# Kernel tuning notes

Measured on AMD Instinct MI355X. Metric: run time of the kernel, lower is better.

Reference implementation:

```python
import jax, jax.numpy as jnp
import numpy as np

D_MODEL = 2048
D_FFN = 8192
TOP_K = 256


def setup_inputs() -> dict:
    key = jax.random.key(0)
    kx, kg, ku, kd = jax.random.split(key, 4)
    B, S = 4, 2048
    x = jax.random.normal(kx, (B, S, D_MODEL), dtype=jnp.float32)
    # kaiming_uniform_(a=sqrt(5)) on a 2D tensor -> U(-1/sqrt(fan_in), 1/sqrt(fan_in)),
    # where PyTorch's fan_in is size(1) of the parameter.
    bg = 1.0 / np.sqrt(D_FFN)
    w_gate = jax.random.uniform(kg, (D_MODEL, D_FFN), jnp.float32, -bg, bg)
    w_up = jax.random.uniform(ku, (D_MODEL, D_FFN), jnp.float32, -bg, bg)
    bd = 1.0 / np.sqrt(D_MODEL)
    w_down = jax.random.uniform(kd, (D_FFN, D_MODEL), jnp.float32, -bd, bd)
    return {"x": x, "w_gate": w_gate, "w_up": w_up, "w_down": w_down}


def reference(x, w_gate, w_up, w_down):
    orig_shape = x.shape
    xf = x.reshape(-1, x.shape[-1])          # [N, d_model]
    G = xf @ w_gate                           # [N, d_ffn]
    U = xf @ w_up                             # [N, d_ffn]
    _, idx = jax.lax.top_k(G, TOP_K)          # [N, k] int32 indices into d_ffn
    Gk = jnp.take_along_axis(G, idx, axis=-1)  # [N, k]
    Uk = jnp.take_along_axis(U, idx, axis=-1)  # [N, k]
    Z = jax.nn.silu(Gk) * Uk                   # fused sparse SiLU activation, [N, k]
    # Sparse-to-dense down projection: scatter the k active channels per token
    # back into d_ffn (top-k indices are unique per row, so .set is exact),
    # then a single dense matmul with w_down.
    N = G.shape[0]
    Zd = jnp.zeros((N, D_FFN), dtype=Z.dtype).at[jnp.arange(N)[:, None], idx].set(Z)
    out = Zd @ w_down                          # [N, d_model]
    return out.reshape(*orig_shape[:-1], w_down.shape[-1])
```

## Files before the change

kernel.cpp:

```cpp
#include <hip/hip_runtime.h>
#include <hip/hip_bf16.h>
#include <stdint.h>

#define D_MODEL 2048
#define D_FFN   8192
#define NTOK    8192
#define TOPK    256

typedef __bf16 bf16x8 __attribute__((ext_vector_type(8)));
typedef __bf16 bf16x4 __attribute__((ext_vector_type(4)));
typedef float  f32x4  __attribute__((ext_vector_type(4)));

__device__ inline void load_lds16(const void* g, void* l) {
    __builtin_amdgcn_global_load_lds((__attribute__((address_space(1))) void*)g,
                                     (__attribute__((address_space(3))) void*)l,
                                     16, 0, 0);
}

template<int NSEG, int SEGK, int LDA, int LDB, int LDC, bool ATOMIC>
__global__ __attribute__((amdgpu_flat_work_group_size(512, 512),
                          amdgpu_waves_per_eu(2)))
void g256p(const __bf16* __restrict__ A0, const __bf16* __restrict__ A1,
           const __bf16* __restrict__ A2,
           const __bf16* __restrict__ B0, const __bf16* __restrict__ B1,
           const __bf16* __restrict__ B2,
           float* __restrict__ C)
{
    constexpr int KEXT = NSEG * SEGK;
    constexpr int NH   = KEXT / 32;
    constexpr int NIT  = NH / 4;

    __shared__ __align__(16) __bf16 sA[4][256][32];
    __shared__ __align__(16) __bf16 sB[4][256][32];

    const int tid  = threadIdx.x;
    const int lane = tid & 63;
    const int wid  = tid >> 6;
    const int mb   = blockIdx.y;
    const int nb   = blockIdx.x;

    const size_t zoff = (size_t)blockIdx.z * KEXT;
    A0 += zoff; B0 += zoff;

    const int wm = (wid >> 2) * 128;
    const int wn = (wid & 3) * 64;
    const int fr = lane & 15;
    const int q  = lane >> 4;

    const int swz8 = ((q ^ ((fr >> 1) & 3)) * 8);
    const int cl   = lane & 3;
    const int sr0  = wid * 32 + (lane >> 2);
    const int cg8a = (cl ^ ((sr0 >> 1) & 3)) * 8;

    f32x4 acc[8][4] = {};

    auto STAGE = [&](int op, int J) {
        const int s = J & 3;
        int seg = 0, kin = J * 32;
        if (NSEG > 1) { seg = (J * 32) / SEGK; kin = J * 32 - seg * SEGK; }
        const __bf16* base = op
            ? ((NSEG == 1 || seg == 0) ? B0 : (seg == 1 ? B1 : B2))
            : ((NSEG == 1 || seg == 0) ? A0 : (seg == 1 ? A1 : A2));
        const int rowbase = (op ? nb : mb) * 256;
        const int ld = op ? LDB : LDA;
        char* ldsb = (char*)(op ? &sB[s][0][0] : &sA[s][0][0]) + wid * 2048;
        #pragma unroll
        for (int p = 0; p < 2; ++p) {
            const int r = sr0 + p * 16;
            load_lds16(base + (size_t)(rowbase + r) * ld + kin + cg8a,
                       ldsb + p * 1024);
        }
    };

#define P_READ_B(s) { _Pragma("unroll") for (int ni = 0; ni < 4; ++ni) {       \
        const int r = wn + fr + ni * 16;                                       \
        bfr[ni] = *(const bf16x8*)&sB[s][r][swz8]; } }
#define P_READ_A(s, h) { _Pragma("unroll") for (int mi = 0; mi < 4; ++mi) {    \
        const int r = wm + (h) * 64 + fr + mi * 16;                            \
        af[mi] = *(const bf16x8*)&sA[s][r][swz8]; } }
#define P_MFMA(h) { __builtin_amdgcn_s_setprio(1);                             \
    _Pragma("unroll") for (int mi = 0; mi < 4; ++mi)                           \
    _Pragma("unroll") for (int ni = 0; ni < 4; ++ni)                           \
        acc[(h) * 4 + mi][ni] = __builtin_amdgcn_mfma_f32_16x16x32_bf16(       \
            af[mi], bfr[ni], acc[(h) * 4 + mi][ni], 0, 0, 0);                  \
    __builtin_amdgcn_s_setprio(0); }
#define P_STAGE2(Joff) { const int J = J0 + (Joff);                            \
        if (J >= 4 && J < NH) { STAGE(0, J); STAGE(1, J); } }
#define P_BAR  __builtin_amdgcn_s_barrier()
#define P_LGKM { asm volatile("s_waitcnt lgkmcnt(0)" ::: "memory");            \
                 __builtin_amdgcn_sched_barrier(0); }
#define SLOT_PHASE(sp, VM) {                                                   \
        P_READ_B(sp); P_READ_A(sp, 0);                                         \
        P_STAGE2(3 + (sp));                                                    \
        P_BAR; P_LGKM;                                                         \
        P_MFMA(0);                                                             \
        __builtin_amdgcn_sched_barrier(0);                                     \
        P_READ_A(sp, 1);                                                       \
        P_LGKM;                                                                \
        P_MFMA(1);                                                             \
        VM;                                                                    \
        P_BAR; }

    #pragma unroll
    for (int J = 0; J < 4; ++J) { STAGE(0, J); STAGE(1, J); }
    asm volatile("s_waitcnt vmcnt(0)" ::: "memory");
    P_BAR;

    for (int i = 0; i < NIT; ++i) {
        const int J0 = 4 * i;
        const bool last = (i == NIT - 1);
        bf16x8 af[4], bfr[4];

        SLOT_PHASE(0, );
        SLOT_PHASE(1,
            if (last) { asm volatile("s_waitcnt vmcnt(0)" ::: "memory"); }
            else      { asm volatile("s_waitcnt vmcnt(4)" ::: "memory"); });
        SLOT_PHASE(2, );
        SLOT_PHASE(3,
            if (last) { asm volatile("s_waitcnt vmcnt(0)" ::: "memory"); }
            else      { asm volatile("s_waitcnt vmcnt(4)" ::: "memory"); });
    }

#undef P_READ_B
#undef P_READ_A
#undef P_MFMA
#undef P_STAGE2
#undef P_BAR
#undef P_LGKM
#undef SLOT_PHASE

    const int orow = q * 4;
    #pragma unroll
    for (int ai = 0; ai < 8; ++ai) {
        const int rl = wm + (ai >> 2) * 64 + (ai & 3) * 16 + orow;
        #pragma unroll
        for (int ni = 0; ni < 4; ++ni)
            #pragma unroll
            for (int j = 0; j < 4; ++j) {
                const int r = mb * 256 + rl + j;
                const int c = nb * 256 + wn + ni * 16 + fr;
                if (ATOMIC)
                    unsafeAtomicAdd(&C[(size_t)r * LDC + c], acc[ai][ni][j]);
                else
                    C[(size_t)r * LDC + c] = acc[ai][ni][j];
            }
    }
}

__global__ __launch_bounds__(256)
void split_convert(const float* __restrict__ in, __bf16* __restrict__ hi,
                   __bf16* __restrict__ lo, int n4)
{
    const int i = blockIdx.x * 256 + threadIdx.x;
    if (i >= n4) return;
    const float4 v = ((const float4*)in)[i];
    float f[4] = {v.x, v.y, v.z, v.w};
    bf16x4 h, l;
    #pragma unroll
    for (int j = 0; j < 4; ++j) {
        __bf16 hb = (__bf16)f[j];
        h[j] = hb;
        l[j] = (__bf16)(f[j] - (float)hb);
    }
    ((bf16x4*)hi)[i] = h;
    ((bf16x4*)lo)[i] = l;
}

template<bool SPLIT>
__global__ __launch_bounds__(256)
void transpose_bf16(const float* __restrict__ in, __bf16* __restrict__ outHi,
                    __bf16* __restrict__ outLo, int R, int C)
{
    __shared__ float tile[32][33];
    const int bx = blockIdx.x * 32;
    const int by = blockIdx.y * 32;
    const int tx = threadIdx.x & 31;
    const int ty = threadIdx.x >> 5;
    #pragma unroll
    for (int i = 0; i < 4; ++i)
        tile[ty + 8 * i][tx] = in[(size_t)(by + ty + 8 * i) * C + (bx + tx)];
    __syncthreads();
    #pragma unroll
    for (int i = 0; i < 4; ++i) {
        const float v = tile[tx][ty + 8 * i];
        const size_t o = (size_t)(bx + ty + 8 * i) * R + (by + tx);
        const __bf16 h = (__bf16)v;
        outHi[o] = h;
        if (SPLIT) outLo[o] = (__bf16)(v - (float)h);
    }
}

#define TK_EPS 3e-5f
#define TK_MAXA 64

__global__ __launch_bounds__(256)
void topk256(const float* __restrict__ G, const float* __restrict__ xblk,
             const float* __restrict__ wgate,
             int* __restrict__ idxOut, float* __restrict__ gkOut)
{
    const int row = blockIdx.x;
    const int t = threadIdx.x;
    const int lane = t & 63;
    const int wid  = t >> 6;

    __shared__ unsigned keys[D_FFN];
    __shared__ float    xr[D_MODEL];
    __shared__ unsigned hist[256];
    __shared__ unsigned scanb[256];
    __shared__ int      sIdx[TOPK];
    __shared__ float    sVal[TOPK];
    __shared__ int      ambIdx[TK_MAXA];
    __shared__ double   ambVal[TK_MAXA];
    __shared__ double   redW[4];
    __shared__ unsigned sh_bin, sh_above, sh_nc, sh_na, sh_fill;

    const float* g = G + (size_t)row * D_FFN;
    const float* xrow = xblk + (size_t)row * D_MODEL;
    for (int i = t; i < D_FFN; i += 256) {
        const unsigned u = __float_as_uint(g[i]);
        keys[i] = (u & 0x80000000u) ? ~u : (u | 0x80000000u);
    }
    for (int i = t; i < D_MODEL; i += 256) xr[i] = xrow[i];
    if (t == 0) { sh_nc = 0; sh_na = 0; sh_fill = 0; }
    __syncthreads();

    unsigned prefix = 0, pmask = 0;
    int remaining = TOPK;
    for (int shift = 24; shift >= 0; shift -= 8) {
        hist[t] = 0;
        __syncthreads();
        for (int i = t; i < D_FFN; i += 256) {
            const unsigned k = keys[i];
            if ((k & pmask) == prefix) atomicAdd(&hist[(k >> shift) & 255u], 1u);
        }
        __syncthreads();
        scanb[t] = hist[t];
        __syncthreads();
        for (int off = 1; off < 256; off <<= 1) {
            const unsigned add = (t + off < 256) ? scanb[t + off] : 0u;
            __syncthreads();
            scanb[t] += add;
            __syncthreads();
        }
        const unsigned above = (t == 255) ? 0u : scanb[t + 1];
        if (scanb[t] >= (unsigned)remaining && above < (unsigned)remaining) {
            sh_bin = (unsigned)t;
            sh_above = above;
        }
        __syncthreads();
        prefix |= sh_bin << shift;
        pmask  |= 0xFFu << shift;
        remaining -= (int)sh_above;
        __syncthreads();
    }
    const unsigned Tkey = prefix;
    const float vT = __uint_as_float((Tkey & 0x80000000u) ? (Tkey & 0x7FFFFFFFu) : ~Tkey);

    for (int i = t; i < D_FFN; i += 256) {
        const unsigned k = keys[i];
        const float f = __uint_as_float((k & 0x80000000u) ? (k & 0x7FFFFFFFu) : ~k);
        if (f > vT + TK_EPS) {
            const unsigned p = atomicAdd(&sh_nc, 1u);
            sIdx[p] = i;
            sVal[p] = f;
        } else if (f >= vT - TK_EPS) {
            const unsigned p = atomicAdd(&sh_na, 1u);
            if (p < TK_MAXA) ambIdx[p] = i;
        }
    }
    __syncthreads();
    const int nc = (int)sh_nc;
    const int na = min((int)sh_na, TK_MAXA);
    const int need = TOPK - nc;

    if (need >= na) {
        if (t < na) {
            const unsigned k = keys[ambIdx[t]];
            sIdx[nc + t] = ambIdx[t];
            sVal[nc + t] = __uint_as_float((k & 0x80000000u) ? (k & 0x7FFFFFFFu) : ~k);
        }
        __syncthreads();
    } else {
        for (int j = 0; j < na; ++j) {
            const int col = ambIdx[j];
            double p = 0.0;
            for (int k = t; k < D_MODEL; k += 256)
                p += (double)xr[k] * (double)wgate[(size_t)k * D_FFN + col];
            #pragma unroll
            for (int o = 32; o > 0; o >>= 1) p += __shfl_xor(p, o, 64);
            if (lane == 0) redW[wid] = p;
            __syncthreads();
            if (t == 0) ambVal[j] = (redW[0] + redW[1]) + (redW[2] + redW[3]);
            __syncthreads();
        }
        if (t < na) {
            const double v = ambVal[t];
            const int    c = ambIdx[t];
            int r = 0;
            for (int j = 0; j < na; ++j) {
                const double vj = ambVal[j];
                if (vj > v || (vj == v && ambIdx[j] < c)) r++;
            }
            if (r < need) {
                const unsigned p = atomicAdd(&sh_fill, 1u);
                sIdx[nc + p] = c;
                sVal[nc + p] = (float)v;
            }
        }
        __syncthreads();
    }

    idxOut[(size_t)row * TOPK + t] = sIdx[t];
    gkOut[(size_t)row * TOPK + t] = sVal[t];
}

__global__ __launch_bounds__(256)
void z_fused(const int* __restrict__ idx, const float* __restrict__ gk,
             const float* __restrict__ U, __bf16* __restrict__ Zd)
{
    const int r = blockIdx.x, t = threadIdx.x;
    const int p = r * TOPK + t;
    const int c = idx[p];
    const float g = gk[p];
    const float u = U[(size_t)r * D_FFN + c];
    const float s = g / (1.0f + __expf(-g));
    Zd[(size_t)r * D_FFN + c] = (__bf16)(s * u);
}

__global__ __launch_bounds__(256)
void zero_buf(float4* __restrict__ p, int n)
{
    int i = blockIdx.x * 256 + threadIdx.x;
    const int stride = gridDim.x * 256;
    for (; i < n; i += stride) p[i] = make_float4(0.f, 0.f, 0.f, 0.f);
}

extern "C" void kernel_launch(void* const* d_in, const int* in_sizes, int n_in,
                              void* d_out, int out_size, void* d_ws, size_t ws_size,
                              hipStream_t stream)
{
    const float* x  = (const float*)d_in[0];
    const float* wg = (const float*)d_in[1];
    const float* wu = (const float*)d_in[2];
    const float* wd = (const float*)d_in[3];
    float* out = (float*)d_out;

    const size_t SZ_XB = (size_t)NTOK * D_MODEL * 2;
    const size_t SZ_WB = (size_t)D_FFN * D_MODEL * 2;
    const size_t SZ_IK = (size_t)NTOK * TOPK * 4;
    char* ws = (char*)d_ws;
    size_t off = 0;
    auto alloc = [&](size_t bytes) -> char* {
        char* p = ws + off;
        off += (bytes + 255) & ~(size_t)255;
        return p;
    };
    __bf16* x_hi  = (__bf16*)alloc(SZ_XB);
    __bf16* x_lo  = (__bf16*)alloc(SZ_XB);
    __bf16* wT_a  = (__bf16*)alloc(SZ_WB);
    __bf16* wT_b  = (__bf16*)alloc(SZ_WB);
    int*    idx   = (int*)  alloc(SZ_IK);
    float*  gk    = (float*)alloc(SZ_IK);
    const size_t fixed = off;

    int RB = 2048;
    while (RB > 256 && fixed + (size_t)RB * D_FFN * 4 > ws_size) RB >>= 1;
    float* Eblk = (float*)alloc((size_t)RB * D_FFN * 4);
    __bf16* Zdb = x_lo;
    const int NRB = NTOK / RB;

    split_convert<<<(NTOK * D_MODEL / 4 + 255) / 256, 256, 0, stream>>>(
        x, x_hi, x_lo, NTOK * D_MODEL / 4);
    transpose_bf16<true><<<dim3(D_FFN / 32, D_MODEL / 32), 256, 0, stream>>>(
        wg, wT_a, wT_b, D_MODEL, D_FFN);

    for (int rb = 0; rb < NRB; ++rb) {
        const size_t aoff = (size_t)rb * RB * D_MODEL;
        g256p<3, D_MODEL, D_MODEL, D_MODEL, D_FFN, false>
            <<<dim3(D_FFN / 256, RB / 256, 1), 512, 0, stream>>>(
                x_hi + aoff, x_lo + aoff, x_hi + aoff,
                wT_a, wT_a, wT_b, Eblk);
        topk256<<<RB, 256, 0, stream>>>(
            Eblk, x + aoff, wg,
            idx + (size_t)rb * RB * TOPK, gk + (size_t)rb * RB * TOPK);
    }

    transpose_bf16<false><<<dim3(D_FFN / 32, D_MODEL / 32), 256, 0, stream>>>(
        wu, wT_a, nullptr, D_MODEL, D_FFN);
    transpose_bf16<false><<<dim3(D_MODEL / 32, D_FFN / 32), 256, 0, stream>>>(
        wd, wT_b, nullptr, D_FFN, D_MODEL);

    zero_buf<<<4096, 256, 0, stream>>>(
        (float4*)out, (int)((size_t)NTOK * D_MODEL * 4 / 16));

    for (int rb = 0; rb < NRB; ++rb) {
        const size_t aoff = (size_t)rb * RB * D_MODEL;
        g256p<1, D_MODEL, D_MODEL, D_MODEL, D_FFN, false>
            <<<dim3(D_FFN / 256, RB / 256, 1), 512, 0, stream>>>(
                x_hi + aoff, nullptr, nullptr, wT_a, nullptr, nullptr, Eblk);
        zero_buf<<<2048, 256, 0, stream>>>((float4*)Zdb, RB * (D_FFN * 2 / 16));
        z_fused<<<RB, 256, 0, stream>>>(
            idx + (size_t)rb * RB * TOPK, gk + (size_t)rb * RB * TOPK, Eblk, Zdb);
        g256p<1, D_MODEL, D_FFN, D_FFN, D_MODEL, true>
            <<<dim3(D_MODEL / 256, RB / 256, D_FFN / D_MODEL), 512, 0, stream>>>(
                Zdb, nullptr, nullptr, wT_b, nullptr, nullptr, out + aoff);
    }
}
```

Baseline: 2.064 ms.

## Store U in bf16, fuse Zd zeroing into scatter, single down-proj GEMM

The up-projection GEMM now writes U as bf16 rather than fp32. Zeroing of the sparse Zd rows moves into the scatter kernel. When the workspace can hold a full bf16 Zd buffer for all tokens, the per-block split-K atomic down projections are replaced by one non-atomic GEMM over all tokens, which also drops the zeroing of the output. This cuts memory traffic, atomic adds and kernel launches, at the cost of a larger workspace footprint and bf16 rounding of U before the activation.

```diff
diff --git a/kernel.cpp b/kernel.cpp
--- a/kernel.cpp
+++ b/kernel.cpp
@@ -17,7 +17,7 @@
                                      16, 0, 0);
 }
 
-template<int NSEG, int SEGK, int LDA, int LDB, int LDC, bool ATOMIC>
+template<int NSEG, int SEGK, int LDA, int LDB, int LDC, bool ATOMIC, bool OUTB16>
 __global__ __attribute__((amdgpu_flat_work_group_size(512, 512),
                           amdgpu_waves_per_eu(2)))
 void g256p(const __bf16* __restrict__ A0, const __bf16* __restrict__ A1,
@@ -139,10 +139,13 @@
             for (int j = 0; j < 4; ++j) {
                 const int r = mb * 256 + rl + j;
                 const int c = nb * 256 + wn + ni * 16 + fr;
+                const float v = acc[ai][ni][j];
                 if (ATOMIC)
-                    unsafeAtomicAdd(&C[(size_t)r * LDC + c], acc[ai][ni][j]);
+                    unsafeAtomicAdd(&C[(size_t)r * LDC + c], v);
+                else if (OUTB16)
+                    ((__bf16*)C)[(size_t)r * LDC + c] = (__bf16)v;
                 else
-                    C[(size_t)r * LDC + c] = acc[ai][ni][j];
+                    C[(size_t)r * LDC + c] = v;
             }
     }
 }
@@ -315,14 +318,19 @@
 }
 
 __global__ __launch_bounds__(256)
-void z_fused(const int* __restrict__ idx, const float* __restrict__ gk,
-             const float* __restrict__ U, __bf16* __restrict__ Zd)
+void z_zero_scatter(const int* __restrict__ idx, const float* __restrict__ gk,
+                    const __bf16* __restrict__ Ub, __bf16* __restrict__ Zd)
 {
     const int r = blockIdx.x, t = threadIdx.x;
+    bf16x8 zv = {};
+    bf16x8* rowv = (bf16x8*)(Zd + (size_t)r * D_FFN);
+    #pragma unroll
+    for (int j = 0; j < 4; ++j) rowv[j * 256 + t] = zv;
+    __syncthreads();
     const int p = r * TOPK + t;
     const int c = idx[p];
     const float g = gk[p];
-    const float u = U[(size_t)r * D_FFN + c];
+    const float u = (float)Ub[(size_t)r * D_FFN + c];
     const float s = g / (1.0f + __expf(-g));
     Zd[(size_t)r * D_FFN + c] = (__bf16)(s * u);
 }
@@ -348,6 +356,7 @@
     const size_t SZ_XB = (size_t)NTOK * D_MODEL * 2;
     const size_t SZ_WB = (size_t)D_FFN * D_MODEL * 2;
     const size_t SZ_IK = (size_t)NTOK * TOPK * 4;
+    const size_t SZ_ZD = (size_t)NTOK * D_FFN * 2;
     char* ws = (char*)d_ws;
     size_t off = 0;
     auto alloc = [&](size_t bytes) -> char* {
@@ -356,17 +365,20 @@
         return p;
     };
     __bf16* x_hi  = (__bf16*)alloc(SZ_XB);
-    __bf16* x_lo  = (__bf16*)alloc(SZ_XB);
     __bf16* wT_a  = (__bf16*)alloc(SZ_WB);
     __bf16* wT_b  = (__bf16*)alloc(SZ_WB);
     int*    idx   = (int*)  alloc(SZ_IK);
     float*  gk    = (float*)alloc(SZ_IK);
-    const size_t fixed = off;
 
     int RB = 2048;
-    while (RB > 256 && fixed + (size_t)RB * D_FFN * 4 > ws_size) RB >>= 1;
-    float* Eblk = (float*)alloc((size_t)RB * D_FFN * 4);
-    __bf16* Zdb = x_lo;
+    while (RB > 256 && off + (size_t)RB * D_FFN * 4 + SZ_XB > ws_size) RB >>= 1;
+    float*  Eblk = (float*)alloc((size_t)RB * D_FFN * 4);
+    const size_t xlo_off = off;
+    __bf16* x_lo = (__bf16*)alloc(SZ_XB);
+    const bool fullZd = (RB == 2048) && (xlo_off + SZ_ZD <= ws_size);
+    __bf16* Zd_full = (__bf16*)(ws + xlo_off);
+    __bf16* Zdb     = x_lo;
+    __bf16* Ub      = (__bf16*)Eblk;
     const int NRB = NTOK / RB;
 
     split_convert<<<(NTOK * D_MODEL / 4 + 255) / 256, 256, 0, stream>>>(
@@ -376,7 +388,7 @@
 
     for (int rb = 0; rb < NRB; ++rb) {
         const size_t aoff = (size_t)rb * RB * D_MODEL;
-        g256p<3, D_MODEL, D_MODEL, D_MODEL, D_FFN, false>
+        g256p<3, D_MODEL, D_MODEL, D_MODEL, D_FFN, false, false>
             <<<dim3(D_FFN / 256, RB / 256, 1), 512, 0, stream>>>(
                 x_hi + aoff, x_lo + aoff, x_hi + aoff,
                 wT_a, wT_a, wT_b, Eblk);
@@ -390,19 +402,33 @@
     transpose_bf16<false><<<dim3(D_MODEL / 32, D_FFN / 32), 256, 0, stream>>>(
         wd, wT_b, nullptr, D_FFN, D_MODEL);
 
-    zero_buf<<<4096, 256, 0, stream>>>(
-        (float4*)out, (int)((size_t)NTOK * D_MODEL * 4 / 16));
-
-    for (int rb = 0; rb < NRB; ++rb) {
-        const size_t aoff = (size_t)rb * RB * D_MODEL;
-        g256p<1, D_MODEL, D_MODEL, D_MODEL, D_FFN, false>
-            <<<dim3(D_FFN / 256, RB / 256, 1), 512, 0, stream>>>(
-                x_hi + aoff, nullptr, nullptr, wT_a, nullptr, nullptr, Eblk);
-        zero_buf<<<2048, 256, 0, stream>>>((float4*)Zdb, RB * (D_FFN * 2 / 16));
-        z_fused<<<RB, 256, 0, stream>>>(
-            idx + (size_t)rb * RB * TOPK, gk + (size_t)rb * RB * TOPK, Eblk, Zdb);
-        g256p<1, D_MODEL, D_FFN, D_FFN, D_MODEL, true>
-            <<<dim3(D_MODEL / 256, RB / 256, D_FFN / D_MODEL), 512, 0, stream>>>(
-                Zdb, nullptr, nullptr, wT_b, nullptr, nullptr, out + aoff);
-    }
-}
+    if (fullZd) {
+        for (int rb = 0; rb < NRB; ++rb) {
+            const size_t aoff = (size_t)rb * RB * D_MODEL;
+            g256p<1, D_MODEL, D_MODEL, D_MODEL, D_FFN, false, true>
+                <<<dim3(D_FFN / 256, RB / 256, 1), 512, 0, stream>>>(
+                    x_hi + aoff, nullptr, nullptr, wT_a, nullptr, nullptr, Eblk);
+            z_zero_scatter<<<RB, 256, 0, stream>>>(
+                idx + (size_t)rb * RB * TOPK, gk + (size_t)rb * RB * TOPK,
+                Ub, Zd_full + (size_t)rb * RB * D_FFN);
+        }
+        g256p<1, D_FFN, D_FFN, D_FFN, D_MODEL, false, false>
+            <<<dim3(D_MODEL / 256, NTOK / 256, 1), 512, 0, stream>>>(
+                Zd_full, nullptr, nullptr, wT_b, nullptr, nullptr, out);
+    } else {
+        zero_buf<<<4096, 256, 0, stream>>>(
+            (float4*)out, (int)((size_t)NTOK * D_MODEL * 4 / 16));
+        for (int rb = 0; rb < NRB; ++rb) {
+            const size_t aoff = (size_t)rb * RB * D_MODEL;
+            g256p<1, D_MODEL, D_MODEL, D_MODEL, D_FFN, false, true>
+                <<<dim3(D_FFN / 256, RB / 256, 1), 512, 0, stream>>>(
+                    x_hi + aoff, nullptr, nullptr, wT_a, nullptr, nullptr, Eblk);
+            z_zero_scatter<<<RB, 256, 0, stream>>>(
+                idx + (size_t)rb * RB * TOPK, gk + (size_t)rb * RB * TOPK,
+                Ub, Zdb);
+            g256p<1, D_MODEL, D_FFN, D_FFN, D_MODEL, true, false>
+                <<<dim3(D_MODEL / 256, RB / 256, D_FFN / D_MODEL), 512, 0, stream>>>(
+                    Zdb, nullptr, nullptr, wT_b, nullptr, nullptr, out + aoff);
+        }
+    }
+}
```

Measured after the change: 2.045 ms. No clear change (-0.9%).
